# Optimization experiments

Measured on AMD Instinct MI355X. Metric: run time of the kernel, lower is better.

The kernel has to match this reference:

```python
import jax, jax.numpy as jnp
import numpy as np


def _norm_adj(edge_index, edge_weights, num_nodes):
    """Faithful port of edge_index2norm_adj: dense scatter + self-loops +
    symmetric degree normalization (deg_inv_sqrt is detached in the original)."""
    row, col = edge_index[0], edge_index[1]
    half = edge_weights * 0.5
    adj = jnp.zeros((num_nodes, num_nodes), dtype=edge_weights.dtype)
    adj = adj.at[row, col].add(half)
    adj = adj.at[col, row].add(half)
    adj = adj + jnp.eye(num_nodes, dtype=adj.dtype)
    deg = adj.sum(axis=1)
    deg_inv_sqrt = jnp.where(deg > 0, jax.lax.rsqrt(deg), 0.0)
    deg_inv_sqrt = jax.lax.stop_gradient(deg_inv_sqrt)  # torch.no_grad + detach
    return deg_inv_sqrt[:, None] * adj * deg_inv_sqrt[None, :]


def setup_inputs() -> dict:
    key = jax.random.key(0)
    k1, k2, k3, k4, k5 = jax.random.split(key, 5)
    N, E, D_IN, D_H, D_OUT = 16384, 524288, 64, 64, 16
    x = jax.random.normal(k1, (N, D_IN), dtype=jnp.float32)
    edge_index = jax.random.randint(k2, (2, E), 0, N, dtype=jnp.int64)
    edge_weights = jax.random.uniform(k3, (E,), dtype=jnp.float32)
    W1 = jax.random.normal(k4, (D_IN, D_H), dtype=jnp.float32) / np.sqrt(D_IN)
    b1 = jnp.zeros((D_H,), dtype=jnp.float32)
    W2 = jax.random.normal(k5, (D_H, D_OUT), dtype=jnp.float32) / np.sqrt(D_H)
    b2 = jnp.zeros((D_OUT,), dtype=jnp.float32)
    return {"x": x, "W1": W1, "b1": b1, "W2": W2, "b2": b2,
            "edge_weights": edge_weights, "edge_index": edge_index}


def reference(x, W1, b1, W2, b2, edge_weights, edge_index):
    num_nodes = x.shape[0]
    A = _norm_adj(edge_index, edge_weights, num_nodes)   # [N, N]
    h = jax.nn.relu(A @ (x @ W1) + b1)                   # GCN layer 1
    out = A @ (h @ W2) + b2                              # GCN layer 2 (logits)
    return out
```

## Files before the change

### kernel.cpp

```cpp
#include <hip/hip_runtime.h>

constexpr int TPB   = 256;
constexpr int NMAX  = 16384;
constexpr int GBMAX = 1024;
constexpr int CHUNK = 2048;



__global__ __launch_bounds__(1024) void k_p1(const int* __restrict__ ei,
    const float* __restrict__ ew, int E, int rsh, int NBe, int GB,
    int* __restrict__ bstartT, int* __restrict__ bcntT, int2* __restrict__ tmp) {
    __shared__ int cnt[256];
    __shared__ int curs[256];
    __shared__ int sc[256];
    __shared__ int2 stg[2 * CHUNK];
    int tid = threadIdx.x;
    int b = blockIdx.x;
    int e0 = b * CHUNK;
    int e1 = min(E, e0 + CHUNK);
    if (tid < NBe) cnt[tid] = 0;
    __syncthreads();
    int ea = e0 + tid, ebg = e0 + 1024 + tid;
    int r0 = 0, c0 = 0, r1 = 0, c1 = 0, w0 = 0, w1 = 0;
    bool va = ea < e1, vb = ebg < e1;
    if (va) { r0 = ei[ea];  c0 = ei[E + ea];  w0 = __float_as_int(0.5f * ew[ea]); }
    if (vb) { r1 = ei[ebg]; c1 = ei[E + ebg]; w1 = __float_as_int(0.5f * ew[ebg]); }
    if (va) { atomicAdd(&cnt[r0 >> rsh], 1); atomicAdd(&cnt[c0 >> rsh], 1); }
    if (vb) { atomicAdd(&cnt[r1 >> rsh], 1); atomicAdd(&cnt[c1 >> rsh], 1); }
    __syncthreads();
    int myc = (tid < NBe) ? cnt[tid] : 0;
    if (tid < NBe) sc[tid] = myc;
    __syncthreads();
    for (int off = 1; off < NBe; off <<= 1) {
        int v = 0;
        if (tid < NBe && tid >= off) v = sc[tid - off];
        __syncthreads();
        if (tid < NBe) sc[tid] += v;
        __syncthreads();
    }
    if (tid < NBe) {
        int excl = sc[tid] - myc;
        curs[tid] = excl;
        bstartT[tid * GB + b] = 2 * e0 + excl;
        bcntT[tid * GB + b] = myc;
    }
    __syncthreads();
    int mask = (1 << rsh) - 1;
    if (va) {
        int p = atomicAdd(&curs[r0 >> rsh], 1);
        stg[p] = make_int2(((r0 & mask) << 20) | c0, w0);
        p = atomicAdd(&curs[c0 >> rsh], 1);
        stg[p] = make_int2(((c0 & mask) << 20) | r0, w0);
    }
    if (vb) {
        int p = atomicAdd(&curs[r1 >> rsh], 1);
        stg[p] = make_int2(((r1 & mask) << 20) | c1, w1);
        p = atomicAdd(&curs[c1 >> rsh], 1);
        stg[p] = make_int2(((c1 & mask) << 20) | r1, w1);
    }
    __syncthreads();
    int tot = 2 * (e1 - e0);
    for (int i = tid; i < tot; i += 1024) tmp[2 * e0 + i] = stg[i];
}

__global__ void k_colsum(const int* __restrict__ bcntT, int GB,
                         int* __restrict__ btot) {
    __shared__ int red[TPB / 64];
    int k = blockIdx.x;
    int s = 0;
    for (int b = threadIdx.x; b < GB; b += TPB) s += bcntT[k * GB + b];
    #pragma unroll
    for (int off = 32; off; off >>= 1) s += __shfl_down(s, off, 64);
    int wv = threadIdx.x >> 6;
    if ((threadIdx.x & 63) == 0) red[wv] = s;
    __syncthreads();
    if (threadIdx.x == 0) {
        int t = 0;
        for (int w = 0; w < TPB / 64; ++w) t += red[w];
        btot[k] = t;
    }
}

__global__ void k_scan256(const int* __restrict__ btot, int NBe,
                          int* __restrict__ entBase, int* __restrict__ rowptr,
                          int N, int M) {
    __shared__ int tot[256];
    int k = threadIdx.x;
    int s = (k < NBe) ? btot[k] : 0;
    tot[k] = s;
    __syncthreads();
    for (int off = 1; off < 256; off <<= 1) {
        int v = (k >= off) ? tot[k - off] : 0;
        __syncthreads();
        tot[k] += v;
        __syncthreads();
    }
    if (k < NBe) entBase[k] = tot[k] - s;
    if (k == 0) rowptr[N] = M;
}

__global__ __launch_bounds__(1024) void k_p2(const int2* __restrict__ tmp,
    const int* __restrict__ bstartT, const int* __restrict__ bcntT,
    const int* __restrict__ entBase, int GB, int rsh, int N,
    int2* __restrict__ ent, int* __restrict__ rowptr, float* __restrict__ dis) {
    __shared__ int ncnt[256];
    __shared__ int nstart[256];
    __shared__ int ncur[256];
    __shared__ float wsum[256];
    int k = blockIdx.x;
    int tid = threadIdx.x;
    int RN = 1 << rsh;
    int n0 = k << rsh;
    if (tid < RN) { ncnt[tid] = 0; wsum[tid] = 0.f; }
    __syncthreads();
    int eb = entBase[k];
    int grp = tid >> 2, sub = tid & 3;
    for (int b = grp; b < GB; b += 256) {
        int s = bstartT[k * GB + b];
        int l = bcntT[k * GB + b];
        for (int u = sub; u < l; u += 4) {
            int2 v = tmp[s + u];
            atomicAdd(&ncnt[v.x >> 20], 1);
        }
    }
    __syncthreads();
    int myc = (tid < RN) ? ncnt[tid] : 0;
    if (tid < RN) nstart[tid] = myc;
    __syncthreads();
    for (int off = 1; off < RN; off <<= 1) {
        int v = 0;
        if (tid < RN && tid >= off) v = nstart[tid - off];
        __syncthreads();
        if (tid < RN) nstart[tid] += v;
        __syncthreads();
    }
    if (tid < RN) { nstart[tid] -= myc; ncur[tid] = nstart[tid]; }
    __syncthreads();
    for (int b = grp; b < GB; b += 256) {
        int s = bstartT[k * GB + b];
        int l = bcntT[k * GB + b];
        for (int u = sub; u < l; u += 4) {
            int2 v = tmp[s + u];
            int rl = v.x >> 20;
            int cc = v.x & 0xFFFFF;
            int p = atomicAdd(&ncur[rl], 1);
            ent[eb + p] = make_int2(cc, v.y);
            atomicAdd(&wsum[rl], __int_as_float(v.y));
        }
    }
    __syncthreads();
    if (tid < RN && n0 + tid < N) {
        rowptr[n0 + tid] = eb + nstart[tid];
        dis[n0 + tid] = rsqrtf(1.f + wsum[tid]);
    }
}

__global__ void k_init_fb(float* deg, int* counts, int N) {
    int i = blockIdx.x * TPB + threadIdx.x;
    if (i < N) { deg[i] = 1.0f; counts[i] = 0; }
}
__global__ void k_deg_cnt_fb(const int* __restrict__ ei, const float* __restrict__ ew,
                             float* deg, int* counts, int E) {
    int e = blockIdx.x * TPB + threadIdx.x;
    if (e >= E) return;
    int r = ei[e], c = ei[E + e];
    float hw = 0.5f * ew[e];
    unsafeAtomicAdd(&deg[r], hw);
    unsafeAtomicAdd(&deg[c], hw);
    atomicAdd(&counts[r], 1);
    atomicAdd(&counts[c], 1);
}
__global__ void k_rsqrt_fb(float* degdis, int N) {
    int i = blockIdx.x * TPB + threadIdx.x;
    if (i < N) {
        float d = degdis[i];
        degdis[i] = d > 0.f ? rsqrtf(d) : 0.f;
    }
}
__global__ void k_scan_fb(const int* __restrict__ counts, int* __restrict__ rowptr,
                          int* __restrict__ cursor, int N) {
    __shared__ int partial[TPB];
    int tid = threadIdx.x;
    int chunk = (N + TPB - 1) / TPB;
    int begin = tid * chunk;
    int end = begin + chunk; if (end > N) end = N;
    int s = 0;
    for (int i = begin; i < end; ++i) s += counts[i];
    partial[tid] = s;
    __syncthreads();
    for (int off = 1; off < TPB; off <<= 1) {
        int v = partial[tid];
        int add = (tid >= off) ? partial[tid - off] : 0;
        __syncthreads();
        partial[tid] = v + add;
        __syncthreads();
    }
    int base = (tid == 0) ? 0 : partial[tid - 1];
    for (int i = begin; i < end; ++i) {
        rowptr[i] = base; cursor[i] = base;
        base += counts[i];
    }
    if (tid == TPB - 1) rowptr[N] = base;
}
__global__ void k_fill_fb(const int* __restrict__ ei, const float* __restrict__ ew,
                          int* cursor, int2* __restrict__ ent, int E) {
    int e = blockIdx.x * TPB + threadIdx.x;
    if (e >= E) return;
    int r = ei[e], c = ei[E + e];
    int hw = __float_as_int(0.5f * ew[e]);
    int p1 = atomicAdd(&cursor[r], 1);
    ent[p1] = make_int2(c, hw);
    int p2 = atomicAdd(&cursor[c], 1);
    ent[p2] = make_int2(r, hw);
}

__global__ void k_gemm1(const float* __restrict__ X, const float* __restrict__ W,
                        const float* __restrict__ dis, float* __restrict__ Z, int N) {
    __shared__ float Wl[64 * 64];
    int tid = threadIdx.x;
    #pragma unroll
    for (int i = tid; i < 4096; i += TPB) Wl[i] = W[i];
    __syncthreads();
    int row = blockIdx.x * 4 + (tid >> 6);
    int f = tid & 63;
    if (row >= N) return;
    const float* xr = X + row * 64;
    float s = 0.f;
    #pragma unroll
    for (int k = 0; k < 64; ++k) s = fmaf(xr[k], Wl[k * 64 + f], s);
    Z[row * 64 + f] = dis[row] * s;
}

template <int D, bool RELU>
__global__ void k_gather(const float* __restrict__ Z, const int* __restrict__ rowptr,
                         const long long* __restrict__ entq, const float* __restrict__ dis,
                         const float* __restrict__ bias, float* __restrict__ out, int N) {
    constexpr int NPB = TPB / D;
    int node = blockIdx.x * NPB + threadIdx.x / D;
    int f = threadIdx.x % D;
    int lane = threadIdx.x & 63;
    int base = lane & ~(D - 1);
    if (node >= N) return;
    int j0 = rowptr[node], j1 = rowptr[node + 1];
    float acc = Z[node * D + f];
    long long cur = 0;
    if (j0 < j1) cur = __builtin_nontemporal_load(entq + j0 + f);
    for (int jb = j0; jb < j1; jb += D) {
        long long nxt = cur;
        if (jb + D < j1) nxt = __builtin_nontemporal_load(entq + jb + D + f);
        int ex = (int)cur;
        float ey = __int_as_float((int)(cur >> 32));
        int cnt = j1 - jb; if (cnt > D) cnt = D;
        int k = 0;
        for (; k + 8 <= cnt; k += 8) {
            int n[8]; float w[8], z[8];
            #pragma unroll
            for (int u = 0; u < 8; ++u) {
                n[u] = __shfl(ex, base + k + u);
                w[u] = __shfl(ey, base + k + u);
            }
            #pragma unroll
            for (int u = 0; u < 8; ++u) z[u] = Z[n[u] * D + f];
            #pragma unroll
            for (int u = 0; u < 8; ++u) acc = fmaf(w[u], z[u], acc);
        }
        for (; k < cnt; ++k) {
            int n0 = __shfl(ex, base + k);
            float w0 = __shfl(ey, base + k);
            acc = fmaf(w0, Z[n0 * D + f], acc);
        }
        cur = nxt;
    }
    float v = fmaf(dis[node], acc, bias[f]);
    if (RELU) v = v > 0.f ? v : 0.f;
    out[node * D + f] = v;
}

__global__ void k_gemm2(const float* __restrict__ H, const float* __restrict__ W2,
                        const float* __restrict__ dis, float* __restrict__ Z2, int N) {
    __shared__ float Wl[64 * 16];
    int tid = threadIdx.x;
    #pragma unroll
    for (int i = tid; i < 1024; i += TPB) Wl[i] = W2[i];
    __syncthreads();
    int row = blockIdx.x * 16 + (tid >> 4);
    int f = tid & 15;
    if (row >= N) return;
    const float* hr = H + row * 64;
    float s = 0.f;
    #pragma unroll
    for (int k = 0; k < 64; ++k) s = fmaf(hr[k], Wl[k * 16 + f], s);
    Z2[row * 16 + f] = dis[row] * s;
}

extern "C" void kernel_launch(void* const* d_in, const int* in_sizes, int n_in,
                              void* d_out, int out_size, void* d_ws, size_t ws_size,
                              hipStream_t stream) {
    const float* x  = (const float*)d_in[0];
    const float* W1 = (const float*)d_in[1];
    const float* b1 = (const float*)d_in[2];
    const float* W2 = (const float*)d_in[3];
    const float* b2 = (const float*)d_in[4];
    const float* ew = (const float*)d_in[5];
    const int*   ei = (const int*)d_in[6];

    const int N = in_sizes[0] / 64;
    const int E = in_sizes[5];
    const int M = 2 * E;

    int rsh = 0;
    while ((256 << rsh) < N) ++rsh;
    const int NBe = (N + (1 << rsh) - 1) >> rsh;
    const int GB  = (E + CHUNK - 1) / CHUNK;

    char* ws = (char*)d_ws;
    size_t off = 0;
    auto alloc = [&](size_t bytes) -> void* {
        void* p = ws + off;
        off += (bytes + 255) & ~(size_t)255;
        return p;
    };
    float* dis     = (float*)alloc((size_t)N * 4);
    int*   counts  = (int*)alloc((size_t)N * 4);
    int*   rowptr  = (int*)alloc(((size_t)N + 1) * 4);
    int*   cursor  = (int*)alloc((size_t)N * 4);
    int2*  ent     = (int2*)alloc(((size_t)M + 64) * 8);
    int*   bstartT = (int*)alloc((size_t)GB * NBe * 4);
    int*   bcntT   = (int*)alloc((size_t)GB * NBe * 4);
    int*   btot    = (int*)alloc(((size_t)NBe + 1) * 4);
    int*   entBase = (int*)alloc(((size_t)NBe + 1) * 4);
    float* Z1      = (float*)alloc((size_t)N * 64 * 4);
    float* H       = (float*)alloc((size_t)N * 64 * 4);
    float* Z2      = (float*)alloc((size_t)N * 16 * 4);
    (void)ws_size; (void)n_in; (void)out_size;

    int2* tmp = (int2*)Z1;

    float* out = (float*)d_out;

    if (N <= NMAX && GB <= GBMAX) {
        k_p1<<<GB, 1024, 0, stream>>>(ei, ew, E, rsh, NBe, GB, bstartT, bcntT, tmp);
        k_colsum<<<NBe, TPB, 0, stream>>>(bcntT, GB, btot);
        k_scan256<<<1, 256, 0, stream>>>(btot, NBe, entBase, rowptr, N, M);
        k_p2<<<NBe, 1024, 0, stream>>>(tmp, bstartT, bcntT, entBase, GB, rsh, N,
                                       ent, rowptr, dis);
    } else {
        k_init_fb<<<(N + TPB - 1) / TPB, TPB, 0, stream>>>(dis, counts, N);
        k_deg_cnt_fb<<<(E + TPB - 1) / TPB, TPB, 0, stream>>>(ei, ew, dis, counts, E);
        k_rsqrt_fb<<<(N + TPB - 1) / TPB, TPB, 0, stream>>>(dis, N);
        k_scan_fb<<<1, TPB, 0, stream>>>(counts, rowptr, cursor, N);
        k_fill_fb<<<(E + TPB - 1) / TPB, TPB, 0, stream>>>(ei, ew, cursor, ent, E);
    }

    k_gemm1<<<(N + 3) / 4, TPB, 0, stream>>>(x, W1, dis, Z1, N);
    k_gather<64, true><<<(N + 3) / 4, TPB, 0, stream>>>(Z1, rowptr, (const long long*)ent,
                                                        dis, b1, H, N);
    k_gemm2<<<(N + 15) / 16, TPB, 0, stream>>>(H, W2, dis, Z2, N);
    k_gather<16, false><<<(N + 15) / 16, TPB, 0, stream>>>(Z2, rowptr, (const long long*)ent,
                                                           dis, b2, out, N);
}
```

Baseline: 156.8 us.

## Vectorize gathers with float4, stage CSR build in LDS, fold scan into p2

The gather kernels now have each lane accumulate a float4, so fewer lanes share each node and more nodes fit per block. The CSR build halves the p1 chunk size and folds the block-total scan into k_p2, removing one launch. k_p2 now stages its segment entries in shared memory so that tmp is read from global memory only once, with an overflow path for buckets larger than the shared buffer. The large shared staging buffer lowers p2 occupancy, and the longer serial per-thread segment loops may hurt load balance.

```diff
diff --git a/kernel.cpp b/kernel.cpp
--- a/kernel.cpp
+++ b/kernel.cpp
@@ -2,8 +2,9 @@
 
 constexpr int TPB   = 256;
 constexpr int NMAX  = 16384;
+constexpr int CHUNK = 1024;
 constexpr int GBMAX = 1024;
-constexpr int CHUNK = 2048;
+constexpr int P2CAP = 10240;
 
 
 
@@ -20,13 +21,14 @@
     int e1 = min(E, e0 + CHUNK);
     if (tid < NBe) cnt[tid] = 0;
     __syncthreads();
-    int ea = e0 + tid, ebg = e0 + 1024 + tid;
-    int r0 = 0, c0 = 0, r1 = 0, c1 = 0, w0 = 0, w1 = 0;
-    bool va = ea < e1, vb = ebg < e1;
-    if (va) { r0 = ei[ea];  c0 = ei[E + ea];  w0 = __float_as_int(0.5f * ew[ea]); }
-    if (vb) { r1 = ei[ebg]; c1 = ei[E + ebg]; w1 = __float_as_int(0.5f * ew[ebg]); }
-    if (va) { atomicAdd(&cnt[r0 >> rsh], 1); atomicAdd(&cnt[c0 >> rsh], 1); }
-    if (vb) { atomicAdd(&cnt[r1 >> rsh], 1); atomicAdd(&cnt[c1 >> rsh], 1); }
+    int e = e0 + tid;
+    bool va = e < e1;
+    int r = 0, c = 0, w = 0;
+    if (va) {
+        r = ei[e]; c = ei[E + e]; w = __float_as_int(0.5f * ew[e]);
+        atomicAdd(&cnt[r >> rsh], 1);
+        atomicAdd(&cnt[c >> rsh], 1);
+    }
     __syncthreads();
     int myc = (tid < NBe) ? cnt[tid] : 0;
     if (tid < NBe) sc[tid] = myc;
@@ -47,16 +49,10 @@
     __syncthreads();
     int mask = (1 << rsh) - 1;
     if (va) {
-        int p = atomicAdd(&curs[r0 >> rsh], 1);
-        stg[p] = make_int2(((r0 & mask) << 20) | c0, w0);
-        p = atomicAdd(&curs[c0 >> rsh], 1);
-        stg[p] = make_int2(((c0 & mask) << 20) | r0, w0);
-    }
-    if (vb) {
-        int p = atomicAdd(&curs[r1 >> rsh], 1);
-        stg[p] = make_int2(((r1 & mask) << 20) | c1, w1);
-        p = atomicAdd(&curs[c1 >> rsh], 1);
-        stg[p] = make_int2(((c1 & mask) << 20) | r1, w1);
+        int p = atomicAdd(&curs[r >> rsh], 1);
+        stg[p] = make_int2(((r & mask) << 20) | c, w);
+        p = atomicAdd(&curs[c >> rsh], 1);
+        stg[p] = make_int2(((c & mask) << 20) | r, w);
     }
     __syncthreads();
     int tot = 2 * (e1 - e0);
@@ -81,47 +77,51 @@
     }
 }
 
-__global__ void k_scan256(const int* __restrict__ btot, int NBe,
-                          int* __restrict__ entBase, int* __restrict__ rowptr,
-                          int N, int M) {
-    __shared__ int tot[256];
-    int k = threadIdx.x;
-    int s = (k < NBe) ? btot[k] : 0;
-    tot[k] = s;
-    __syncthreads();
-    for (int off = 1; off < 256; off <<= 1) {
-        int v = (k >= off) ? tot[k - off] : 0;
-        __syncthreads();
-        tot[k] += v;
-        __syncthreads();
-    }
-    if (k < NBe) entBase[k] = tot[k] - s;
-    if (k == 0) rowptr[N] = M;
-}
-
 __global__ __launch_bounds__(1024) void k_p2(const int2* __restrict__ tmp,
     const int* __restrict__ bstartT, const int* __restrict__ bcntT,
-    const int* __restrict__ entBase, int GB, int rsh, int N,
+    const int* __restrict__ btot, int GB, int rsh, int N, int NBe, int M,
     int2* __restrict__ ent, int* __restrict__ rowptr, float* __restrict__ dis) {
-    __shared__ int ncnt[256];
-    __shared__ int nstart[256];
-    __shared__ int ncur[256];
-    __shared__ float wsum[256];
+    __shared__ int sco[256];
+    __shared__ int segoff[GBMAX];
+    __shared__ int ncnt[64];
+    __shared__ int nstart[64];
+    __shared__ int ncur[64];
+    __shared__ float wsum[64];
+    __shared__ int2 stg[P2CAP];
     int k = blockIdx.x;
     int tid = threadIdx.x;
     int RN = 1 << rsh;
     int n0 = k << rsh;
+    int bt = (tid < NBe) ? btot[tid] : 0;
+    if (tid < 256) sco[tid] = bt;
+    __syncthreads();
+    for (int off = 1; off < 256; off <<= 1) {
+        int v = 0;
+        if (tid < 256 && tid >= off) v = sco[tid - off];
+        __syncthreads();
+        if (tid < 256) sco[tid] += v;
+        __syncthreads();
+    }
+    int btotk = btot[k];
+    int eb = sco[k] - btotk;
     if (tid < RN) { ncnt[tid] = 0; wsum[tid] = 0.f; }
-    __syncthreads();
-    int eb = entBase[k];
-    int grp = tid >> 2, sub = tid & 3;
-    for (int b = grp; b < GB; b += 256) {
-        int s = bstartT[k * GB + b];
-        int l = bcntT[k * GB + b];
-        for (int u = sub; u < l; u += 4) {
-            int2 v = tmp[s + u];
-            atomicAdd(&ncnt[v.x >> 20], 1);
-        }
+    int l = (tid < GB) ? bcntT[k * GB + tid] : 0;
+    int s = (tid < GB) ? bstartT[k * GB + tid] : 0;
+    if (tid < GB) segoff[tid] = l;
+    __syncthreads();
+    for (int off = 1; off < GB; off <<= 1) {
+        int v = 0;
+        if (tid < GB && tid >= off) v = segoff[tid - off];
+        __syncthreads();
+        if (tid < GB) segoff[tid] += v;
+        __syncthreads();
+    }
+    int excl = (tid < GB) ? (segoff[tid] - l) : 0;
+    for (int u = 0; u < l; ++u) {
+        int2 v = tmp[s + u];
+        atomicAdd(&ncnt[v.x >> 20], 1);
+        int pos = excl + u;
+        if (pos < P2CAP) stg[pos] = v;
     }
     __syncthreads();
     int myc = (tid < RN) ? ncnt[tid] : 0;
@@ -136,16 +136,26 @@
     }
     if (tid < RN) { nstart[tid] -= myc; ncur[tid] = nstart[tid]; }
     __syncthreads();
-    for (int b = grp; b < GB; b += 256) {
-        int s = bstartT[k * GB + b];
-        int l = bcntT[k * GB + b];
-        for (int u = sub; u < l; u += 4) {
-            int2 v = tmp[s + u];
-            int rl = v.x >> 20;
-            int cc = v.x & 0xFFFFF;
-            int p = atomicAdd(&ncur[rl], 1);
-            ent[eb + p] = make_int2(cc, v.y);
-            atomicAdd(&wsum[rl], __int_as_float(v.y));
+    int staged = min(btotk, P2CAP);
+    for (int i = tid; i < staged; i += 1024) {
+        int2 v = stg[i];
+        int rl = v.x >> 20;
+        int cc = v.x & 0xFFFFF;
+        int p = atomicAdd(&ncur[rl], 1);
+        ent[eb + p] = make_int2(cc, v.y);
+        atomicAdd(&wsum[rl], __int_as_float(v.y));
+    }
+    if (btotk > P2CAP && excl + l > P2CAP) {
+        for (int u = 0; u < l; ++u) {
+            int pos = excl + u;
+            if (pos >= P2CAP) {
+                int2 v = tmp[s + u];
+                int rl = v.x >> 20;
+                int cc = v.x & 0xFFFFF;
+                int p = atomicAdd(&ncur[rl], 1);
+                ent[eb + p] = make_int2(cc, v.y);
+                atomicAdd(&wsum[rl], __int_as_float(v.y));
+            }
         }
     }
     __syncthreads();
@@ -153,6 +163,7 @@
         rowptr[n0 + tid] = eb + nstart[tid];
         dis[n0 + tid] = rsqrtf(1.f + wsum[tid]);
     }
+    if (k == 0 && tid == 0) rowptr[N] = M;
 }
 
 __global__ void k_init_fb(float* deg, int* counts, int N) {
@@ -235,45 +246,68 @@
 __global__ void k_gather(const float* __restrict__ Z, const int* __restrict__ rowptr,
                          const long long* __restrict__ entq, const float* __restrict__ dis,
                          const float* __restrict__ bias, float* __restrict__ out, int N) {
-    constexpr int NPB = TPB / D;
-    int node = blockIdx.x * NPB + threadIdx.x / D;
-    int f = threadIdx.x % D;
-    int lane = threadIdx.x & 63;
-    int base = lane & ~(D - 1);
+    constexpr int LPN = D / 4;
+    constexpr int UN = (LPN >= 8) ? 8 : LPN;
+    int tid = threadIdx.x;
+    int lane = tid & 63;
+    int node = blockIdx.x * (TPB / LPN) + tid / LPN;
+    int fq = lane & (LPN - 1);
+    int base = lane - fq;
     if (node >= N) return;
     int j0 = rowptr[node], j1 = rowptr[node + 1];
-    float acc = Z[node * D + f];
+    const float4* Z4 = (const float4*)Z;
+    float4 acc = Z4[node * LPN + fq];
     long long cur = 0;
-    if (j0 < j1) cur = __builtin_nontemporal_load(entq + j0 + f);
-    for (int jb = j0; jb < j1; jb += D) {
+    if (j0 < j1) cur = __builtin_nontemporal_load(entq + j0 + fq);
+    for (int jb = j0; jb < j1; jb += LPN) {
         long long nxt = cur;
-        if (jb + D < j1) nxt = __builtin_nontemporal_load(entq + jb + D + f);
+        if (jb + LPN < j1) nxt = __builtin_nontemporal_load(entq + jb + LPN + fq);
         int ex = (int)cur;
         float ey = __int_as_float((int)(cur >> 32));
-        int cnt = j1 - jb; if (cnt > D) cnt = D;
+        int cnt = j1 - jb; if (cnt > LPN) cnt = LPN;
         int k = 0;
-        for (; k + 8 <= cnt; k += 8) {
-            int n[8]; float w[8], z[8];
+        for (; k + UN <= cnt; k += UN) {
+            int n[UN]; float w[UN]; float4 z[UN];
             #pragma unroll
-            for (int u = 0; u < 8; ++u) {
+            for (int u = 0; u < UN; ++u) {
                 n[u] = __shfl(ex, base + k + u);
                 w[u] = __shfl(ey, base + k + u);
             }
             #pragma unroll
-            for (int u = 0; u < 8; ++u) z[u] = Z[n[u] * D + f];
+            for (int u = 0; u < UN; ++u) z[u] = Z4[n[u] * LPN + fq];
             #pragma unroll
-            for (int u = 0; u < 8; ++u) acc = fmaf(w[u], z[u], acc);
+            for (int u = 0; u < UN; ++u) {
+                acc.x = fmaf(w[u], z[u].x, acc.x);
+                acc.y = fmaf(w[u], z[u].y, acc.y);
+                acc.z = fmaf(w[u], z[u].z, acc.z);
+                acc.w = fmaf(w[u], z[u].w, acc.w);
+            }
         }
         for (; k < cnt; ++k) {
             int n0 = __shfl(ex, base + k);
             float w0 = __shfl(ey, base + k);
-            acc = fmaf(w0, Z[n0 * D + f], acc);
+            float4 z = Z4[n0 * LPN + fq];
+            acc.x = fmaf(w0, z.x, acc.x);
+            acc.y = fmaf(w0, z.y, acc.y);
+            acc.z = fmaf(w0, z.z, acc.z);
+            acc.w = fmaf(w0, z.w, acc.w);
         }
         cur = nxt;
     }
-    float v = fmaf(dis[node], acc, bias[f]);
-    if (RELU) v = v > 0.f ? v : 0.f;
-    out[node * D + f] = v;
+    float d = dis[node];
+    float4 bb = ((const float4*)bias)[fq];
+    float4 v;
+    v.x = fmaf(d, acc.x, bb.x);
+    v.y = fmaf(d, acc.y, bb.y);
+    v.z = fmaf(d, acc.z, bb.z);
+    v.w = fmaf(d, acc.w, bb.w);
+    if (RELU) {
+        v.x = v.x > 0.f ? v.x : 0.f;
+        v.y = v.y > 0.f ? v.y : 0.f;
+        v.z = v.z > 0.f ? v.z : 0.f;
+        v.w = v.w > 0.f ? v.w : 0.f;
+    }
+    ((float4*)out)[node * LPN + fq] = v;
 }
 
 __global__ void k_gemm2(const float* __restrict__ H, const float* __restrict__ W2,
@@ -328,7 +362,6 @@
     int*   bstartT = (int*)alloc((size_t)GB * NBe * 4);
     int*   bcntT   = (int*)alloc((size_t)GB * NBe * 4);
     int*   btot    = (int*)alloc(((size_t)NBe + 1) * 4);
-    int*   entBase = (int*)alloc(((size_t)NBe + 1) * 4);
     float* Z1      = (float*)alloc((size_t)N * 64 * 4);
     float* H       = (float*)alloc((size_t)N * 64 * 4);
     float* Z2      = (float*)alloc((size_t)N * 16 * 4);
@@ -338,11 +371,10 @@
 
     float* out = (float*)d_out;
 
-    if (N <= NMAX && GB <= GBMAX) {
+    if (N <= NMAX && GB <= GBMAX && (size_t)16 * E <= (size_t)512 * N) {
         k_p1<<<GB, 1024, 0, stream>>>(ei, ew, E, rsh, NBe, GB, bstartT, bcntT, tmp);
         k_colsum<<<NBe, TPB, 0, stream>>>(bcntT, GB, btot);
-        k_scan256<<<1, 256, 0, stream>>>(btot, NBe, entBase, rowptr, N, M);
-        k_p2<<<NBe, 1024, 0, stream>>>(tmp, bstartT, bcntT, entBase, GB, rsh, N,
+        k_p2<<<NBe, 1024, 0, stream>>>(tmp, bstartT, bcntT, btot, GB, rsh, N, NBe, M,
                                        ent, rowptr, dis);
     } else {
         k_init_fb<<<(N + TPB - 1) / TPB, TPB, 0, stream>>>(dis, counts, N);
@@ -353,9 +385,9 @@
     }
 
     k_gemm1<<<(N + 3) / 4, TPB, 0, stream>>>(x, W1, dis, Z1, N);
-    k_gather<64, true><<<(N + 3) / 4, TPB, 0, stream>>>(Z1, rowptr, (const long long*)ent,
-                                                        dis, b1, H, N);
+    k_gather<64, true><<<(N + 15) / 16, TPB, 0, stream>>>(Z1, rowptr, (const long long*)ent,
+                                                          dis, b1, H, N);
     k_gemm2<<<(N + 15) / 16, TPB, 0, stream>>>(H, W2, dis, Z2, N);
-    k_gather<16, false><<<(N + 15) / 16, TPB, 0, stream>>>(Z2, rowptr, (const long long*)ent,
+    k_gather<16, false><<<(N + 63) / 64, TPB, 0, stream>>>(Z2, rowptr, (const long long*)ent,
                                                            dis, b2, out, N);
 }
```

After: 162.9 us. 1.04x slower.
